# Kernel optimization log

Hardware: AMD Instinct MI355X
Metric: run time of the kernel (lower is better)

Reference implementation:

```python
import jax, jax.numpy as jnp
import numpy as np

T = 3              # num_ntype (slots)
NH = 64            # num_hidden == num_classes
HEADS = (4, 4, 1)
NUM_ETYPES = 5
EDGE_DIM = 64
N_NODES = 20000
NEG_SLOPE = 0.2
ALPHA = 0.05       # residual-attention blend
EPS = 1e-12


def _l2_by_slot(x):
    # l2_norm with l2BySlot='True': normalize each ntype slot independently
    n = x.shape[0]
    xs = x.reshape(n, T, -1)
    nrm = jnp.linalg.norm(xs, axis=2, keepdims=True)
    return (xs / jnp.maximum(nrm, EPS)).reshape(n, -1)


def _edge_softmax(logits, dst, n):
    # softmax over incoming edges of each destination node
    m = jax.lax.stop_gradient(jax.ops.segment_max(logits, dst, num_segments=n))
    e = jnp.exp(logits - m[dst])
    s = jax.ops.segment_sum(e, dst, num_segments=n)
    return e / s[dst]


def _conv(x, src, dst, etype, W, al, ar, ee_tab, We, ae, res_attn, act):
    # slotGATConv: x [N,T,C], W [T,C,H*O], al/ar [H,T*O], ee_tab [R,De], We [De,H*De], ae [H,De]
    n = x.shape[0]
    H = al.shape[0]
    proj = jnp.einsum('ntc,tcd->ntd', x, W)                     # [N,T,H*O]
    O = proj.shape[-1] // H
    feat = proj.reshape(n, T, H, O).transpose(0, 2, 1, 3).reshape(n, H, T * O)
    el = jnp.einsum('nhd,hd->nh', feat, al)
    er = jnp.einsum('nhd,hd->nh', feat, ar)
    De = ee_tab.shape[1]
    ep = (ee_tab[etype] @ We).reshape(-1, H, De)                # [E,H,De]
    ee = jnp.einsum('ehd,hd->eh', ep, ae)                       # [E,H]
    logit = jax.nn.leaky_relu(el[src] + er[dst] + ee, NEG_SLOPE)
    a = _edge_softmax(logit, dst, n)                            # [E,H]
    if res_attn is not None:
        a = a * (1.0 - ALPHA) + res_attn * ALPHA
    out = jax.ops.segment_sum(feat[src] * a[:, :, None], dst, num_segments=n)  # [N,H,T*O]
    if act:
        out = jax.nn.elu(out)
    return out, a


def _forward(feat0, feat1, feat2, w_in0, b_in0, w_in1, b_in1, w_in2, b_in2,
             l0_W, l0_al, l0_ar, l0_ee, l0_we, l0_ae,
             l1_W, l1_al, l1_ar, l1_ee, l1_we, l1_ae,
             l2_W, l2_al, l2_ar, l2_ee, l2_we, l2_ae,
             dm_W, e_feat, src, dst, left, right, mid):
    feats = [feat0, feat1, feat2]
    lins = [(w_in0, b_in0), (w_in1, b_in1), (w_in2, b_in2)]
    blocks = []
    for t, (f, (w, b)) in enumerate(zip(feats, lins)):
        ft = f @ w + b                                          # [n_t, NH]
        pad = jnp.zeros((f.shape[0], T * NH), ft.dtype)
        blocks.append(pad.at[:, t * NH:(t + 1) * NH].set(ft))   # slot zero-padding
    h = jnp.concatenate(blocks, 0)                              # [N, T*NH]
    emb = [_l2_by_slot(h)]                                      # aggregator='None' -> identity
    x = h.reshape(-1, T, NH)
    out0, a0 = _conv(x, src, dst, e_feat, l0_W, l0_al, l0_ar, l0_ee, l0_we, l0_ae, None, True)
    emb.append(_l2_by_slot(out0.mean(1)))
    x = out0.reshape(-1, HEADS[0], T, NH).transpose(0, 2, 1, 3).reshape(-1, T, HEADS[0] * NH)
    out1, a1 = _conv(x, src, dst, e_feat, l1_W, l1_al, l1_ar, l1_ee, l1_we, l1_ae, a0, True)
    emb.append(_l2_by_slot(out1.mean(1)))
    x = out1.reshape(-1, HEADS[1], T, NH).transpose(0, 2, 1, 3).reshape(-1, T, HEADS[1] * NH)
    out2, _ = _conv(x, src, dst, e_feat, l2_W, l2_al, l2_ar, l2_ee, l2_we, l2_ae, a1, False)
    emb.append(_l2_by_slot(out2.mean(1)))
    # aggregator='None' + inProcessEmb='True': concat per-slot along feature dim
    embs = [e.reshape(-1, T, NH) for e in emb]
    o = jnp.concatenate(embs, 2).reshape(-1, T * NH * len(embs))  # [N, 768]
    le, re = o[left], o[right]
    scores = jnp.zeros(left.shape[0], o.dtype)
    for r in range(NUM_ETYPES):                                 # DistMult per relation
        s = ((le @ dm_W[r]) * re).sum(1)
        scores = jnp.where(mid == r, s, scores)
    return jax.nn.sigmoid(scores)


def setup_inputs() -> dict:
    key = jax.random.key(0)
    ks = iter(jax.random.split(key, 64))
    def nrm(shape, std):
        return jax.random.normal(next(ks), shape, jnp.float32) * std
    counts = [8000, 6000, 6000]
    in_dims = [256, 128, 64]
    inp = {}
    for t in range(T):
        inp[f'feat{t}'] = jax.random.normal(next(ks), (counts[t], in_dims[t]), jnp.float32)
        inp[f'w_in{t}'] = nrm((in_dims[t], NH), 0.1)
        inp[f'b_in{t}'] = nrm((NH,), 0.1)
    Cs = [NH, HEADS[0] * NH, HEADS[1] * NH]
    for l in range(3):
        H = HEADS[l]
        inp[f'l{l}_W'] = nrm((T, Cs[l], H * NH), 0.1)
        inp[f'l{l}_al'] = nrm((H, T * NH), 0.1)
        inp[f'l{l}_ar'] = nrm((H, T * NH), 0.1)
        inp[f'l{l}_ee'] = nrm((NUM_ETYPES, EDGE_DIM), 0.1)
        inp[f'l{l}_we'] = nrm((EDGE_DIM, H * EDGE_DIM), 0.1)
        inp[f'l{l}_ae'] = nrm((H, EDGE_DIM), 0.1)
    D = T * NH * 4
    inp['dm_W'] = nrm((NUM_ETYPES, D, D), 0.05)
    E, L = 200000, 10000
    inp['e_feat'] = jax.random.randint(next(ks), (E,), 0, NUM_ETYPES)
    inp['src'] = jax.random.randint(next(ks), (E,), 0, N_NODES)
    inp['dst'] = jax.random.randint(next(ks), (E,), 0, N_NODES)
    inp['left'] = jax.random.randint(next(ks), (L,), 0, N_NODES)
    inp['right'] = jax.random.randint(next(ks), (L,), 0, N_NODES)
    inp['mid'] = jax.random.randint(next(ks), (L,), 0, NUM_ETYPES)
    return inp


def reference(feat0, feat1, feat2, w_in0, b_in0, w_in1, b_in1, w_in2, b_in2,
              l0_W, l0_al, l0_ar, l0_ee, l0_we, l0_ae,
              l1_W, l1_al, l1_ar, l1_ee, l1_we, l1_ae,
              l2_W, l2_al, l2_ar, l2_ee, l2_we, l2_ae,
              dm_W, e_feat, src, dst, left, right, mid):
    return _forward(feat0, feat1, feat2, w_in0, b_in0, w_in1, b_in1, w_in2, b_in2,
                    l0_W, l0_al, l0_ar, l0_ee, l0_we, l0_ae,
                    l1_W, l1_al, l1_ar, l1_ee, l1_we, l1_ae,
                    l2_W, l2_al, l2_ar, l2_ee, l2_we, l2_ae,
                    dm_W, e_feat, src, dst, left, right, mid)
```

## Files before the change

kernel.cpp:

```cpp
#include <hip/hip_runtime.h>
#include <math.h>

#define N_NODES 20000
#define NPAD    20096
#define N_EDGES 200000
#define N_PAIRS 10000
#define PAIR_PAD 10368
#define DM_TILES 162
#define NBLK    79

typedef __attribute__((ext_vector_type(8))) short s16x8;
typedef __attribute__((ext_vector_type(4))) float f32x4;

__device__ inline float wave_max(float v){
  for (int o = 32; o > 0; o >>= 1) v = fmaxf(v, __shfl_xor(v, o));
  return v;
}
__device__ inline float wave_sum(float v){
  for (int o = 32; o > 0; o >>= 1) v += __shfl_xor(v, o);
  return v;
}
__device__ inline short f2bf(float x){
  union { float f; unsigned u; } v; v.f = x;
  unsigned r = (v.u + 0x7FFFu + ((v.u >> 16) & 1u)) >> 16;
  return (short)r;
}
__device__ inline float bf2f(short s){
  union { unsigned u; float f; } v; v.u = ((unsigned)(unsigned short)s) << 16;
  return v.f;
}

__global__ void build_h(const float* __restrict__ f0, const float* __restrict__ w0, const float* __restrict__ b0,
                        const float* __restrict__ f1, const float* __restrict__ w1, const float* __restrict__ b1,
                        const float* __restrict__ f2, const float* __restrict__ w2, const float* __restrict__ b2,
                        short* __restrict__ Xb0, short* __restrict__ o_b,
                        int* __restrict__ csr_cnt, int* __restrict__ cnt5, int* __restrict__ pos5,
                        float* __restrict__ score, int* __restrict__ pairs,
                        float* __restrict__ eall, short* __restrict__ Xb12,
                        short* __restrict__ featb){
  const int blk = blockIdx.x, lane = threadIdx.x;
  const int gid = blk * 64 + lane;
  if (gid < N_NODES) csr_cnt[gid] = 0;
  if (gid < 5){ cnt5[gid * 16] = 0; pos5[gid * 16] = 0; }
  if (gid < 10016) score[gid] = 0.f;
  if (gid < PAIR_PAD) pairs[gid] = -1;
  for (int i = gid; i < 480000; i += 160000) eall[i] = 0.f;
  s16x8 z = {};
  if (gid < 4608){
    int t = (gid * 16) / 24576, off = (gid * 16) % 24576;
    short* p = Xb12 + ((size_t)(t * NPAD + N_NODES)) * 256 + off;
    *(s16x8*)p = z; *(s16x8*)(p + 8) = z;
  }
  if (gid < 1152){
    int t = (gid * 16) / 6144, off = (gid * 16) % 6144;
    short* p = Xb0 + ((size_t)(t * NPAD + N_NODES)) * 64 + off;
    *(s16x8*)p = z; *(s16x8*)(p + 8) = z;
  }
  int t, C, nbase; const float *f, *w, *b;
  if (blk < 1000)       { t = 0; nbase = 0;     C = 256; f = f0; w = w0; b = b0; }
  else if (blk < 1750)  { t = 1; nbase = 8000;  C = 128; f = f1; w = w1; b = b1; }
  else                  { t = 2; nbase = 14000; C = 64;  f = f2; w = w2; b = b2; }
  const int n0 = blk * 8;
  const int n0l = n0 - nbase;
  __shared__ float xs[8 * 256];
  const float* fr = f + (size_t)n0l * C;
  for (int i = lane; i < 8 * C; i += 64) xs[i] = fr[i];
  __syncthreads();
  float acc[8];
#pragma unroll
  for (int j = 0; j < 8; j++) acc[j] = b[lane];
  for (int c = 0; c < C; c++){
    float wv = w[c * 64 + lane];
#pragma unroll
    for (int j = 0; j < 8; j++) acc[j] += xs[j * C + c] * wv;
  }
  for (int j = 0; j < 8; j++){
    int n = n0 + j;
    {
      int h = lane >> 4, si = (lane >> 3) & 1, j8 = lane & 7;
      int s0 = (t == 0) ? 1 : 0;
      int s1 = (t == 2) ? 1 : 2;
      int toff = si ? s1 : s0;
      *(s16x8*)(featb + ((size_t)n * 4 + h) * 192 + toff * 64 + j8 * 8) = z;
    }
    for (int tt = 0; tt < 3; tt++)
      Xb0[((size_t)(tt * NPAD) + n) * 64 + lane] = f2bf((tt == t) ? acc[j] : 0.f);
    float ss = wave_sum(acc[j] * acc[j]);
    float sc = 1.f / fmaxf(sqrtf(ss), 1e-12f);
    for (int tt = 0; tt < 3; tt++)
      o_b[(size_t)n * 768 + tt * 256 + lane] = f2bf((tt == t) ? acc[j] * sc : 0.f);
  }
}

__global__ void count_prep_k(const int* __restrict__ dst, int* __restrict__ csr_cnt,
                             const int* __restrict__ mid, int* __restrict__ cnt5,
                             const float* __restrict__ lW0, const float* __restrict__ lW1,
                             const float* __restrict__ lW2, const float* __restrict__ dmW,
                             short* __restrict__ Wt0, short* __restrict__ Wt1,
                             short* __restrict__ Wt2, short* __restrict__ Mt,
                             const float* __restrict__ ee0, const float* __restrict__ we0, const float* __restrict__ ae0,
                             const float* __restrict__ ee1, const float* __restrict__ we1, const float* __restrict__ ae1,
                             const float* __restrict__ ee2, const float* __restrict__ we2, const float* __restrict__ ae2,
                             float* __restrict__ ee5f){
  if (blockIdx.x < 782){
    int e = blockIdx.x * 256 + threadIdx.x;
    int lane = threadIdx.x & 63;
    if (e < N_EDGES) atomicAdd(&csr_cnt[dst[e]], 1);
    int r_mine = (e < N_PAIRS) ? mid[e] : -1;
#pragma unroll
    for (int r = 0; r < 5; r++){
      unsigned long long mask = __ballot(r_mine == r);
      if (mask){
        int leader = __ffsll((long long)mask) - 1;
        if (lane == leader) atomicAdd(&cnt5[r * 16], __popcll(mask));
      }
    }
    return;
  }
  int lin = blockIdx.x - 782;
  int z = lin / 576;
  int rem = lin % 576;
  int by = rem / 24, bx = rem % 24;
  if (z == 10){
    int r = bx, L = by;
    if (r >= 5 || L >= 3) return;
    int H = (L == 2) ? 1 : 4;
    const float* eetab = (L == 0) ? ee0 : ((L == 1) ? ee1 : ee2);
    const float* We    = (L == 0) ? we0 : ((L == 1) ? we1 : we2);
    const float* ae    = (L == 0) ? ae0 : ((L == 1) ? ae1 : ae2);
    int h = threadIdx.x >> 6, lane = threadIdx.x & 63;
    if (h >= H) return;
    float v = 0.f;
    for (int k = 0; k < 64; k++) v += eetab[r * 64 + k] * We[k * H * 64 + h * 64 + lane];
    v *= ae[h * 64 + lane];
    v = wave_sum(v);
    if (lane == 0) ee5f[L * 32 + r * H + h] = v;
    return;
  }
  const float* s; short* d; int R, Cc, r0, c0;
  if (z < 5){
    s = dmW + (size_t)z * 589824; d = Mt + (size_t)z * 589824;
    R = 768; Cc = 768; r0 = bx * 32; c0 = by * 32;
  } else if (z < 8){
    if (bx >= 8 || by >= 8) return;
    int t = z - 5;
    s = lW1 + (size_t)t * 65536; d = Wt1 + (size_t)t * 65536;
    R = 256; Cc = 256; r0 = bx * 32; c0 = by * 32;
  } else if (z == 8){
    if (bx >= 6 || by >= 8) return;
    int t = bx >> 1;
    s = lW0 + (size_t)t * 16384; d = Wt0 + (size_t)t * 16384;
    R = 64; Cc = 256; r0 = (bx & 1) * 32; c0 = by * 32;
  } else {
    if (bx >= 8 || by >= 6) return;
    int t = by >> 1;
    s = lW2 + (size_t)t * 16384; d = Wt2 + (size_t)t * 16384;
    R = 256; Cc = 64; r0 = bx * 32; c0 = (by & 1) * 32;
  }
  __shared__ float tile[32][33];
  int tx = threadIdx.x & 31, ty = threadIdx.x >> 5;
  for (int i = 0; i < 32; i += 8){
    int r = r0 + ty + i;
    tile[ty + i][tx] = (r < R && c0 + tx < Cc) ? s[(size_t)r * Cc + c0 + tx] : 0.f;
  }
  __syncthreads();
  for (int i = 0; i < 32; i += 8){
    int c = c0 + ty + i;
    if (c < Cc && r0 + tx < R)
      d[(size_t)c * R + r0 + tx] = f2bf(tile[tx][ty + i]);
  }
}

__global__ void scan1_k(const int* __restrict__ cnt, int* __restrict__ loc, int* __restrict__ bsum){
  __shared__ int s[256];
  int tid = threadIdx.x;
  int idx = blockIdx.x * 256 + tid;
  int v = (idx < N_NODES) ? cnt[idx] : 0;
  s[tid] = v;
  __syncthreads();
  for (int o = 1; o < 256; o <<= 1){
    int u = (tid >= o) ? s[tid - o] : 0;
    __syncthreads();
    s[tid] += u;
    __syncthreads();
  }
  if (idx < N_NODES) loc[idx] = s[tid] - v;
  if (tid == 255) bsum[blockIdx.x] = s[255];
}

__global__ void scan2_k(const int* __restrict__ bsum, int* __restrict__ bofs,
                        const int* __restrict__ cnt5, int* __restrict__ off5){
  __shared__ int s[128];
  int tid = threadIdx.x;
  int v = (tid < NBLK) ? bsum[tid] : 0;
  s[tid] = v;
  __syncthreads();
  for (int o = 1; o < 128; o <<= 1){
    int u = (tid >= o) ? s[tid - o] : 0;
    __syncthreads();
    s[tid] += u;
    __syncthreads();
  }
  if (tid < NBLK) bofs[tid] = s[tid] - v;
  if (tid == 0){
    int r0 = 0;
    for (int r = 0; r < 5; r++){ off5[r] = r0; r0 += ((cnt5[r * 16] + 63) >> 6) << 6; }
  }
}

__global__ void scan3_k(const int* __restrict__ loc, const int* __restrict__ bofs,
                        int* __restrict__ coff, int* __restrict__ cpos){
  int idx = blockIdx.x * 256 + threadIdx.x;
  if (idx < N_NODES){
    int v = loc[idx] + bofs[blockIdx.x];
    coff[idx] = v;
    cpos[idx * 16] = v;
  }
  if (idx == 0) coff[N_NODES] = N_EDGES;
}

__global__ void scatter_k(const int* __restrict__ dst, const int* __restrict__ srcv,
                          const int* __restrict__ efeat, int* __restrict__ cpos,
                          int* __restrict__ src_sorted, int* __restrict__ et_sorted,
                          const int* __restrict__ mid, const int* __restrict__ off5,
                          int* __restrict__ pos5, int* __restrict__ pairs){
  int e = blockIdx.x * 256 + threadIdx.x;
  int lane = threadIdx.x & 63;
  if (e < N_EDGES){
    int p = atomicAdd(&cpos[dst[e] * 16], 1);
    src_sorted[p] = srcv[e];
    et_sorted[p] = efeat[e];
  }
  int r_mine = (e < N_PAIRS) ? mid[e] : -1;
#pragma unroll
  for (int r = 0; r < 5; r++){
    unsigned long long mask = __ballot(r_mine == r);
    if (mask){
      int cnt = __popcll(mask);
      int leader = __ffsll((long long)mask) - 1;
      int base = 0;
      if (lane == leader) base = atomicAdd(&pos5[r * 16], cnt);
      base = __shfl(base, leader);
      if (r_mine == r){
        int rank = __popcll(mask & ((1ull << lane) - 1ull));
        pairs[off5[r] + base + rank] = e;
      }
    }
  }
}

template<int C, int NO, int TYPED>
__global__ void mfma_proj(const short* __restrict__ Xb, const short* __restrict__ Wt,
                          short* __restrict__ featb, const float* __restrict__ al,
                          const float* __restrict__ ar, float* __restrict__ elf,
                          float* __restrict__ erf){
  constexpr int H = NO / 64;
  const int ct = blockIdx.y;
  const int t  = blockIdx.z;
  int tile = blockIdx.x;
  if (TYPED){
    const int lo[3] = {0, 62, 109};
    const int hi[3] = {63, 110, 157};
    tile += lo[t];
    if (tile >= hi[t]) return;
  }
  const int n0 = tile * 128;
  const int tid = threadIdx.x;
  const int w = tid >> 6, lane = tid & 63;
  const int quad = lane >> 4, ln = lane & 15;
  __shared__ __attribute__((aligned(16))) short A_s[128 * 32];
  __shared__ __attribute__((aligned(16))) short B_s[64 * 32];
  const short* Xt  = Xb + (size_t)t * NPAD * C;
  const short* Wtt = Wt + ((size_t)t * NO + ct * 64) * C;
  f32x4 acc[2][4] = {};
  for (int kk = 0; kk < C; kk += 32){
    {
      int row = tid >> 1, half = tid & 1;
      const s16x8* g = (const s16x8*)(Xt + (size_t)(n0 + row) * C + kk + half * 16);
      s16x8 v0 = g[0], v1 = g[1];
      *(s16x8*)(A_s + row * 32 + half * 16) = v0;
      *(s16x8*)(A_s + row * 32 + half * 16 + 8) = v1;
    }
    {
      int row = tid >> 2, chunk = tid & 3;
      s16x8 v = *(const s16x8*)(Wtt + (size_t)row * C + kk + chunk * 8);
      *(s16x8*)(B_s + row * 32 + chunk * 8) = v;
    }
    __syncthreads();
    s16x8 af0 = *(s16x8*)(A_s + (w * 32 + ln) * 32 + quad * 8);
    s16x8 af1 = *(s16x8*)(A_s + (w * 32 + 16 + ln) * 32 + quad * 8);
    s16x8 bf[4];
#pragma unroll
    for (int b = 0; b < 4; b++) bf[b] = *(s16x8*)(B_s + (b * 16 + ln) * 32 + quad * 8);
#pragma unroll
    for (int b = 0; b < 4; b++){
      acc[0][b] = __builtin_amdgcn_mfma_f32_16x16x32_bf16(af0, bf[b], acc[0][b], 0, 0, 0);
      acc[1][b] = __builtin_amdgcn_mfma_f32_16x16x32_bf16(af1, bf[b], acc[1][b], 0, 0, 0);
    }
    __syncthreads();
  }
#pragma unroll
  for (int ar_ = 0; ar_ < 2; ar_++){
#pragma unroll
    for (int i = 0; i < 4; i++){
      int n = n0 + w * 32 + ar_ * 16 + quad * 4 + i;
      if (n >= N_NODES) continue;
#pragma unroll
      for (int b = 0; b < 4; b++){
        int jj = b * 16 + ln;
        featb[((size_t)n * H + ct) * 192 + t * 64 + jj] = f2bf(acc[ar_][b][i]);
      }
    }
  }
  float alv[4], arv[4];
#pragma unroll
  for (int b = 0; b < 4; b++){
    alv[b] = al[ct * 192 + t * 64 + b * 16 + ln];
    arv[b] = ar[ct * 192 + t * 64 + b * 16 + ln];
  }
#pragma unroll
  for (int ar_ = 0; ar_ < 2; ar_++){
#pragma unroll
    for (int i = 0; i < 4; i++){
      float pe = 0.f, pr = 0.f;
#pragma unroll
      for (int b = 0; b < 4; b++){
        pe += acc[ar_][b][i] * alv[b];
        pr += acc[ar_][b][i] * arv[b];
      }
#pragma unroll
      for (int o = 1; o < 16; o <<= 1){
        pe += __shfl_xor(pe, o);
        pr += __shfl_xor(pr, o);
      }
      int n = n0 + w * 32 + ar_ * 16 + quad * 4 + i;
      if (ln == 0 && n < N_NODES){
        atomicAdd(&elf[n * H + ct], pe);
        atomicAdd(&erf[n * H + ct], pr);
      }
    }
  }
}

template<int H, int MODE, int ACT>
__global__ __launch_bounds__(256) void gat_fused(
    const int* __restrict__ csr_off, const int* __restrict__ src_sorted,
    const int* __restrict__ et_sorted,
    const float* __restrict__ el, const float* __restrict__ er, const float* __restrict__ ee5,
    const float* __restrict__ aprev, float* __restrict__ aout,
    const short* __restrict__ featb, short* __restrict__ outb,
    short* __restrict__ o_b, int kslice){
  const int wid = threadIdx.x >> 6, lane = threadIdx.x & 63;
  const int n = blockIdx.x * 4 + wid;
  if (n >= N_NODES) return;
  constexpr int NC = H * 192 / 8;
  const int c0 = lane, h0 = (c0 / 24) % H;
  const int c1 = lane + 64, h1 = (c1 / 24) % H;
  const bool act0 = (c0 < NC);
  const bool act1 = (H == 4) && (lane < 32);
  const int off = csr_off[n];
  const int cnt = csr_off[n + 1] - off;
  __shared__ float a_s[4][64][H];
  __shared__ float out_s[4][H * 192];
  float acc0[8] = {}, acc1[8] = {};
  float ern[H];
#pragma unroll
  for (int h = 0; h < H; h++) ern[h] = er[n * H + h];

  if (cnt > 0 && cnt <= 64){
    int p = off + lane;
    int sidx = 0, r = 0;
    if (lane < cnt){ sidx = src_sorted[p]; r = et_sorted[p]; }
    float lg[H];
#pragma unroll
    for (int h = 0; h < H; h++) lg[h] = -1e30f;
    if (lane < cnt){
#pragma unroll
      for (int h = 0; h < H; h++){
        float v = el[sidx * H + h] + ern[h] + ee5[r * H + h];
        lg[h] = (v >= 0.f) ? v : 0.2f * v;
      }
    }
    float ap[4] = {};
    if (MODE > 0 && lane < cnt){
#pragma unroll
      for (int q = 0; q < 4; q++) ap[q] = aprev[(size_t)p * 4 + q];
    }
    float av[H];
#pragma unroll
    for (int h = 0; h < H; h++){
      float mh = wave_max(lg[h]);
      float ex = (lane < cnt) ? __expf(lg[h] - mh) : 0.f;
      float sh = wave_sum(ex);
      float a = ex / sh;
      if (MODE == 1) a = 0.95f * a + 0.05f * ap[h];
      if (MODE == 2) a = 0.95f * a + 0.0125f * (ap[0] + ap[1] + ap[2] + ap[3]);
      av[h] = a;
      if (lane < cnt) a_s[wid][lane][h] = a;
    }
    if (MODE != 2 && lane < cnt){
      f32x4 o = {av[0], av[1], av[2], av[3]};
      *(f32x4*)(aout + (size_t)p * 4) = o;
    }
    int b = 0;
    for (; b + 4 <= cnt; b += 4){
      int p4 = off + b;
      int s0 = src_sorted[p4],     s1 = src_sorted[p4 + 1];
      int s2 = src_sorted[p4 + 2], s3 = src_sorted[p4 + 3];
      s16x8 v00, v01, v02, v03, v10, v11, v12, v13;
      if (act0){
        v00 = *(const s16x8*)(featb + (size_t)s0 * (H * 192) + c0 * 8);
        v01 = *(const s16x8*)(featb + (size_t)s1 * (H * 192) + c0 * 8);
        v02 = *(const s16x8*)(featb + (size_t)s2 * (H * 192) + c0 * 8);
        v03 = *(const s16x8*)(featb + (size_t)s3 * (H * 192) + c0 * 8);
      }
      if (act1){
        v10 = *(const s16x8*)(featb + (size_t)s0 * (H * 192) + c1 * 8);
        v11 = *(const s16x8*)(featb + (size_t)s1 * (H * 192) + c1 * 8);
        v12 = *(const s16x8*)(featb + (size_t)s2 * (H * 192) + c1 * 8);
        v13 = *(const s16x8*)(featb + (size_t)s3 * (H * 192) + c1 * 8);
      }
      if (act0){
        float a0 = a_s[wid][b][h0], a1 = a_s[wid][b + 1][h0];
        float a2 = a_s[wid][b + 2][h0], a3 = a_s[wid][b + 3][h0];
#pragma unroll
        for (int i = 0; i < 8; i++)
          acc0[i] += a0 * bf2f(v00[i]) + a1 * bf2f(v01[i]) +
                     a2 * bf2f(v02[i]) + a3 * bf2f(v03[i]);
      }
      if (act1){
        float a0 = a_s[wid][b][h1], a1 = a_s[wid][b + 1][h1];
        float a2 = a_s[wid][b + 2][h1], a3 = a_s[wid][b + 3][h1];
#pragma unroll
        for (int i = 0; i < 8; i++)
          acc1[i] += a0 * bf2f(v10[i]) + a1 * bf2f(v11[i]) +
                     a2 * bf2f(v12[i]) + a3 * bf2f(v13[i]);
      }
    }
    for (; b < cnt; b++){
      int pp = off + b;
      int s = src_sorted[pp];
      if (act0){
        float a = a_s[wid][b][h0];
        s16x8 v = *(const s16x8*)(featb + (size_t)s * (H * 192) + c0 * 8);
#pragma unroll
        for (int i = 0; i < 8; i++) acc0[i] += a * bf2f(v[i]);
      }
      if (act1){
        float a = a_s[wid][b][h1];
        s16x8 v = *(const s16x8*)(featb + (size_t)s * (H * 192) + c1 * 8);
#pragma unroll
        for (int i = 0; i < 8; i++) acc1[i] += a * bf2f(v[i]);
      }
    }
  } else if (cnt > 64){
    float mh[H], sh[H];
#pragma unroll
    for (int h = 0; h < H; h++){ mh[h] = -1e30f; sh[h] = 0.f; }
    for (int b = lane; b < cnt; b += 64){
      int p = off + b; int s = src_sorted[p]; int r = et_sorted[p];
#pragma unroll
      for (int h = 0; h < H; h++){
        float v = el[s * H + h] + ern[h] + ee5[r * H + h];
        v = (v >= 0.f) ? v : 0.2f * v;
        mh[h] = fmaxf(mh[h], v);
      }
    }
#pragma unroll
    for (int h = 0; h < H; h++) mh[h] = wave_max(mh[h]);
    for (int b = lane; b < cnt; b += 64){
      int p = off + b; int s = src_sorted[p]; int r = et_sorted[p];
#pragma unroll
      for (int h = 0; h < H; h++){
        float v = el[s * H + h] + ern[h] + ee5[r * H + h];
        v = (v >= 0.f) ? v : 0.2f * v;
        sh[h] += __expf(v - mh[h]);
      }
    }
#pragma unroll
    for (int h = 0; h < H; h++) sh[h] = wave_sum(sh[h]);
    if (MODE != 2){
      for (int b = lane; b < cnt; b += 64){
        int p = off + b; int s = src_sorted[p]; int r = et_sorted[p];
        float ap[4] = {};
        if (MODE > 0){
#pragma unroll
          for (int q = 0; q < 4; q++) ap[q] = aprev[(size_t)p * 4 + q];
        }
        float av[4] = {};
#pragma unroll
        for (int h = 0; h < H; h++){
          float v = el[s * H + h] + ern[h] + ee5[r * H + h];
          v = (v >= 0.f) ? v : 0.2f * v;
          float a = __expf(v - mh[h]) / sh[h];
          if (MODE == 1) a = 0.95f * a + 0.05f * ap[h];
          av[h] = a;
        }
        f32x4 o = {av[0], av[1], av[2], av[3]};
        *(f32x4*)(aout + (size_t)p * 4) = o;
      }
    }
    for (int b = 0; b < cnt; b++){
      int p = off + b; int s = src_sorted[p]; int r = et_sorted[p];
      const short* row = featb + (size_t)s * (H * 192);
      float apm[4] = {};
      if (MODE > 0){
#pragma unroll
        for (int q = 0; q < 4; q++) apm[q] = aprev[(size_t)p * 4 + q];
      }
      if (act0){
        float v = el[s * H + h0] + ern[h0] + ee5[r * H + h0];
        v = (v >= 0.f) ? v : 0.2f * v;
        float a = __expf(v - mh[h0]) / sh[h0];
        if (MODE == 1) a = 0.95f * a + 0.05f * apm[h0];
        if (MODE == 2) a = 0.95f * a + 0.0125f * (apm[0] + apm[1] + apm[2] + apm[3]);
        s16x8 vv = *(const s16x8*)(row + c0 * 8);
#pragma unroll
        for (int i = 0; i < 8; i++) acc0[i] += a * bf2f(vv[i]);
      }
      if (act1){
        float v = el[s * H + h1] + ern[h1] + ee5[r * H + h1];
        v = (v >= 0.f) ? v : 0.2f * v;
        float a = __expf(v - mh[h1]) / sh[h1];
        if (MODE == 1) a = 0.95f * a + 0.05f * apm[h1];
        s16x8 vv = *(const s16x8*)(row + c1 * 8);
#pragma unroll
        for (int i = 0; i < 8; i++) acc1[i] += a * bf2f(vv[i]);
      }
    }
  }
  if (act0){
    int dd = c0 * 8, h = dd / 192, rr = dd % 192, t = rr / 64, j = rr % 64;
    if (ACT){
#pragma unroll
      for (int i = 0; i < 8; i++) acc0[i] = (acc0[i] > 0.f) ? acc0[i] : expm1f(acc0[i]);
    }
#pragma unroll
    for (int i = 0; i < 8; i++) out_s[wid][dd + i] = acc0[i];
    if (outb){
      s16x8 o;
#pragma unroll
      for (int i = 0; i < 8; i++) o[i] = f2bf(acc0[i]);
      *(s16x8*)(outb + ((size_t)(t * NPAD) + n) * 256 + h * 64 + j) = o;
    }
  }
  if (act1){
    int dd = c1 * 8, h = dd / 192, rr = dd % 192, t = rr / 64, j = rr % 64;
    if (ACT){
#pragma unroll
      for (int i = 0; i < 8; i++) acc1[i] = (acc1[i] > 0.f) ? acc1[i] : expm1f(acc1[i]);
    }
#pragma unroll
    for (int i = 0; i < 8; i++) out_s[wid][dd + i] = acc1[i];
    if (outb){
      s16x8 o;
#pragma unroll
      for (int i = 0; i < 8; i++) o[i] = f2bf(acc1[i]);
      *(s16x8*)(outb + ((size_t)(t * NPAD) + n) * 256 + h * 64 + j) = o;
    }
  }
  for (int t = 0; t < 3; t++){
    float v;
    if (H == 4)
      v = 0.25f * (out_s[wid][t * 64 + lane] + out_s[wid][192 + t * 64 + lane] +
                   out_s[wid][384 + t * 64 + lane] + out_s[wid][576 + t * 64 + lane]);
    else
      v = out_s[wid][t * 64 + lane];
    float ss = wave_sum(v * v);
    float sc = 1.f / fmaxf(sqrtf(ss), 1e-12f);
    o_b[(size_t)n * 768 + t * 256 + kslice * 64 + lane] = f2bf(v * sc);
  }
}

__global__ void distmult_mfma(const short* __restrict__ o_b, const short* __restrict__ Mt,
                              const int* __restrict__ pairs, const int* __restrict__ left,
                              const int* __restrict__ right, const int* __restrict__ mid,
                              float* __restrict__ score){
  const int pt = blockIdx.x, ct = blockIdx.y;
  const int tid = threadIdx.x;
  const int w = tid >> 6, lane = tid & 63;
  const int quad = lane >> 4, ln = lane & 15;
  __shared__ __attribute__((aligned(16))) short smem[8192];
  short* A_s = smem;
  short* B_s = smem + 2048;
  __shared__ int pid_s[64];
  __shared__ int lbase[64];
  if (tid < 64){
    int p = pairs[pt * 64 + tid];
    pid_s[tid] = p;
    lbase[tid] = (p >= 0) ? left[p] * 768 : 0;
  }
  __syncthreads();
  int p0 = pid_s[0];
  if (p0 < 0) return;
  const int r = mid[p0];
  const short* Mr = Mt + (size_t)r * 768 * 768;
  f32x4 acc[8] = {};
  for (int kk = 0; kk < 768; kk += 32){
    {
      int row = tid >> 2, chunk = tid & 3;
      s16x8 v = *(const s16x8*)(o_b + (size_t)lbase[row] + kk + chunk * 8);
      *(s16x8*)(A_s + row * 32 + chunk * 8) = v;
    }
    {
      int row = tid >> 1, half = tid & 1;
      const s16x8* g = (const s16x8*)(Mr + (size_t)(ct * 128 + row) * 768 + kk + half * 16);
      s16x8 v0 = g[0], v1 = g[1];
      *(s16x8*)(B_s + row * 32 + half * 16) = v0;
      *(s16x8*)(B_s + row * 32 + half * 16 + 8) = v1;
    }
    __syncthreads();
    s16x8 af = *(s16x8*)(A_s + (w * 16 + ln) * 32 + quad * 8);
#pragma unroll
    for (int b = 0; b < 8; b++){
      s16x8 bf = *(s16x8*)(B_s + (b * 16 + ln) * 32 + quad * 8);
      acc[b] = __builtin_amdgcn_mfma_f32_16x16x32_bf16(af, bf, acc[b], 0, 0, 0);
    }
    __syncthreads();
  }
  short* RE_s = smem;
  {
    int row = tid >> 2, quarter = tid & 3;
    int p = pid_s[row];
    s16x8 v0 = {}, v1 = {}, v2 = {}, v3 = {};
    if (p >= 0){
      const s16x8* g = (const s16x8*)(o_b + (size_t)right[p] * 768 + ct * 128 + quarter * 32);
      v0 = g[0]; v1 = g[1]; v2 = g[2]; v3 = g[3];
    }
    __syncthreads();
    short* dst = RE_s + row * 128 + quarter * 32;
    *(s16x8*)(dst)      = v0;
    *(s16x8*)(dst + 8)  = v1;
    *(s16x8*)(dst + 16) = v2;
    *(s16x8*)(dst + 24) = v3;
  }
  __syncthreads();
#pragma unroll
  for (int i = 0; i < 4; i++){
    int row = w * 16 + quad * 4 + i;
    float s = 0.f;
#pragma unroll
    for (int b = 0; b < 8; b++)
      s += acc[b][i] * bf2f(RE_s[row * 128 + b * 16 + ln]);
    s += __shfl_xor(s, 1); s += __shfl_xor(s, 2);
    s += __shfl_xor(s, 4); s += __shfl_xor(s, 8);
    if (ln == 0){
      int p = pid_s[row];
      if (p >= 0) atomicAdd(&score[p], s);
    }
  }
}

__global__ void sigmoid_k(const float* __restrict__ score, float* __restrict__ out){
  int i = blockIdx.x * 256 + threadIdx.x;
  if (i < N_PAIRS) out[i] = 1.f / (1.f + __expf(-score[i]));
}

extern "C" void kernel_launch(void* const* d_in, const int* in_sizes, int n_in,
                              void* d_out, int out_size, void* d_ws, size_t ws_size,
                              hipStream_t stream){
  const float* f0 = (const float*)d_in[0];
  const float* w0 = (const float*)d_in[1];
  const float* b0 = (const float*)d_in[2];
  const float* f1 = (const float*)d_in[3];
  const float* w1 = (const float*)d_in[4];
  const float* b1 = (const float*)d_in[5];
  const float* f2 = (const float*)d_in[6];
  const float* w2_ = (const float*)d_in[7];
  const float* b2 = (const float*)d_in[8];
  const float* lW[3]  = {(const float*)d_in[9],  (const float*)d_in[15], (const float*)d_in[21]};
  const float* lal[3] = {(const float*)d_in[10], (const float*)d_in[16], (const float*)d_in[22]};
  const float* lar[3] = {(const float*)d_in[11], (const float*)d_in[17], (const float*)d_in[23]};
  const float* lee[3] = {(const float*)d_in[12], (const float*)d_in[18], (const float*)d_in[24]};
  const float* lwe[3] = {(const float*)d_in[13], (const float*)d_in[19], (const float*)d_in[25]};
  const float* lae[3] = {(const float*)d_in[14], (const float*)d_in[20], (const float*)d_in[26]};
  const float* dmW = (const float*)d_in[27];
  const int* efeat = (const int*)d_in[28];
  const int* srcv  = (const int*)d_in[29];
  const int* dstv  = (const int*)d_in[30];
  const int* left  = (const int*)d_in[31];
  const int* right = (const int*)d_in[32];
  const int* midv  = (const int*)d_in[33];
  float* out = (float*)d_out;

  short* feat_b = (short*)d_ws;
  float* aA     = (float*)(feat_b + 15360000);
  float* aB     = aA + 800000;
  float* eall   = aB + 800000;
  float* ee5f   = eall + 480000;
  float* score  = ee5f + 96;
  int* csr_cnt  = (int*)(score + 10016);
  int* csr_off  = csr_cnt + 20000;
  int* csr_pos  = csr_off + 20004;
  int* loc      = csr_pos + 320000;
  int* bsum     = loc + 20000;
  int* bofs     = bsum + 128;
  int* src_sorted = bofs + 128;
  int* et_sorted  = src_sorted + 200000;
  int* cnt5     = et_sorted + 200000;
  int* off5     = cnt5 + 80;
  int* pos5     = off5 + 8;
  int* pairs    = pos5 + 80;
  short* o_b    = (short*)(pairs + PAIR_PAD);
  short* Xb0    = o_b + 15360000;
  short* Xb12   = Xb0 + 3858432;
  short* Wt0    = Xb12 + 15433728;
  short* Wt1    = Wt0 + 49152;
  short* Wt2    = Wt1 + 196608;
  short* Mt     = Wt2 + 49152;
  float* elf0 = eall, *erf0 = eall + 80000;
  float* elf1 = eall + 160000, *erf1 = eall + 240000;
  float* elf2 = eall + 320000, *erf2 = eall + 400000;

  build_h<<<2500, 64, 0, stream>>>(f0, w0, b0, f1, w1, b1, f2, w2_, b2, Xb0, o_b,
                                   csr_cnt, cnt5, pos5, score, pairs, eall, Xb12, feat_b);
  count_prep_k<<<782 + 6336, 256, 0, stream>>>(dstv, csr_cnt, midv, cnt5,
                                               lW[0], lW[1], lW[2], dmW, Wt0, Wt1, Wt2, Mt,
                                               lee[0], lwe[0], lae[0], lee[1], lwe[1], lae[1],
                                               lee[2], lwe[2], lae[2], ee5f);
  scan1_k<<<NBLK, 256, 0, stream>>>(csr_cnt, loc, bsum);
  scan2_k<<<1, 128, 0, stream>>>(bsum, bofs, cnt5, off5);
  scan3_k<<<NBLK, 256, 0, stream>>>(loc, bofs, csr_off, csr_pos);
  scatter_k<<<782, 256, 0, stream>>>(dstv, srcv, efeat, csr_pos, src_sorted, et_sorted,
                                     midv, off5, pos5, pairs);

  { dim3 g(64, 4, 3);
    mfma_proj<64, 256, 1><<<g, 256, 0, stream>>>(Xb0, Wt0, feat_b, lal[0], lar[0], elf0, erf0); }
  gat_fused<4, 0, 1><<<5000, 256, 0, stream>>>(csr_off, src_sorted, et_sorted, elf0, erf0, ee5f,
                                               nullptr, aA, feat_b, Xb12, o_b, 1);

  { dim3 g(NPAD / 128, 4, 3);
    mfma_proj<256, 256, 0><<<g, 256, 0, stream>>>(Xb12, Wt1, feat_b, lal[1], lar[1], elf1, erf1); }
  gat_fused<4, 1, 1><<<5000, 256, 0, stream>>>(csr_off, src_sorted, et_sorted, elf1, erf1, ee5f + 32,
                                               aA, aB, feat_b, Xb12, o_b, 2);

  { dim3 g(NPAD / 128, 1, 3);
    mfma_proj<256, 64, 0><<<g, 256, 0, stream>>>(Xb12, Wt2, feat_b, lal[2], lar[2], elf2, erf2); }
  gat_fused<1, 2, 0><<<5000, 256, 0, stream>>>(csr_off, src_sorted, et_sorted, elf2, erf2, ee5f + 64,
                                               aB, nullptr, feat_b, nullptr, o_b, 3);

  { dim3 g(DM_TILES, 6); distmult_mfma<<<g, 256, 0, stream>>>(o_b, Mt, pairs, left, right, midv, score); }
  sigmoid_k<<<40, 256, 0, stream>>>(score, out);
}
```

Measured before the change: 509.3 us.

## Sort CSR edges by source node type and skip zero slots in layer-0 aggregation

Edges within each destination's CSR segment are now grouped by the source node's type, using per-(dst,type) counts and cursors. In layer 0 the projected features are nonzero only in the source's own type slot, so the typed aggregation path gathers just that 64-wide slot per head instead of all three. The other paths are also reworked: source indices are cached in shared memory, edge loops are split across half-waves and combined with cross-lane reductions, and the H=1 path is vectorised over 8 edges. Reductions and the ELU/output store are moved into a common shared-memory epilogue. The typed path depends on the node-type boundaries hardcoded at 8000 and 14000.

```diff
diff --git a/kernel.cpp b/kernel.cpp
--- a/kernel.cpp
+++ b/kernel.cpp
@@ -29,18 +29,19 @@
   union { unsigned u; float f; } v; v.u = ((unsigned)(unsigned short)s) << 16;
   return v.f;
 }
+__device__ inline int ntype(int s){ return (s < 8000) ? 0 : ((s < 14000) ? 1 : 2); }
 
 __global__ void build_h(const float* __restrict__ f0, const float* __restrict__ w0, const float* __restrict__ b0,
                         const float* __restrict__ f1, const float* __restrict__ w1, const float* __restrict__ b1,
                         const float* __restrict__ f2, const float* __restrict__ w2, const float* __restrict__ b2,
                         short* __restrict__ Xb0, short* __restrict__ o_b,
-                        int* __restrict__ csr_cnt, int* __restrict__ cnt5, int* __restrict__ pos5,
+                        int* __restrict__ cnt3, int* __restrict__ cnt5, int* __restrict__ pos5,
                         float* __restrict__ score, int* __restrict__ pairs,
                         float* __restrict__ eall, short* __restrict__ Xb12,
                         short* __restrict__ featb){
   const int blk = blockIdx.x, lane = threadIdx.x;
   const int gid = blk * 64 + lane;
-  if (gid < N_NODES) csr_cnt[gid] = 0;
+  if (gid < 80000) cnt3[gid] = 0;
   if (gid < 5){ cnt5[gid * 16] = 0; pos5[gid * 16] = 0; }
   if (gid < 10016) score[gid] = 0.f;
   if (gid < PAIR_PAD) pairs[gid] = -1;
@@ -92,7 +93,8 @@
   }
 }
 
-__global__ void count_prep_k(const int* __restrict__ dst, int* __restrict__ csr_cnt,
+__global__ void count_prep_k(const int* __restrict__ dst, const int* __restrict__ srcv,
+                             int* __restrict__ cnt3,
                              const int* __restrict__ mid, int* __restrict__ cnt5,
                              const float* __restrict__ lW0, const float* __restrict__ lW1,
                              const float* __restrict__ lW2, const float* __restrict__ dmW,
@@ -105,7 +107,10 @@
   if (blockIdx.x < 782){
     int e = blockIdx.x * 256 + threadIdx.x;
     int lane = threadIdx.x & 63;
-    if (e < N_EDGES) atomicAdd(&csr_cnt[dst[e]], 1);
+    if (e < N_EDGES){
+      int tt = ntype(srcv[e]);
+      atomicAdd(&cnt3[dst[e] * 4 + tt], 1);
+    }
     int r_mine = (e < N_PAIRS) ? mid[e] : -1;
 #pragma unroll
     for (int r = 0; r < 5; r++){
@@ -171,11 +176,11 @@
   }
 }
 
-__global__ void scan1_k(const int* __restrict__ cnt, int* __restrict__ loc, int* __restrict__ bsum){
+__global__ void scan1_k(const int* __restrict__ cnt3, int* __restrict__ loc, int* __restrict__ bsum){
   __shared__ int s[256];
   int tid = threadIdx.x;
   int idx = blockIdx.x * 256 + tid;
-  int v = (idx < N_NODES) ? cnt[idx] : 0;
+  int v = (idx < N_NODES) ? (cnt3[idx * 4] + cnt3[idx * 4 + 1] + cnt3[idx * 4 + 2]) : 0;
   s[tid] = v;
   __syncthreads();
   for (int o = 1; o < 256; o <<= 1){
@@ -209,12 +214,16 @@
 }
 
 __global__ void scan3_k(const int* __restrict__ loc, const int* __restrict__ bofs,
-                        int* __restrict__ coff, int* __restrict__ cpos){
+                        int* __restrict__ coff, int* __restrict__ cpos,
+                        const int* __restrict__ cnt3){
   int idx = blockIdx.x * 256 + threadIdx.x;
   if (idx < N_NODES){
     int v = loc[idx] + bofs[blockIdx.x];
     coff[idx] = v;
-    cpos[idx * 16] = v;
+    int c0 = cnt3[idx * 4], c1 = cnt3[idx * 4 + 1];
+    cpos[idx * 4]     = v;
+    cpos[idx * 4 + 1] = v + c0;
+    cpos[idx * 4 + 2] = v + c0 + c1;
   }
   if (idx == 0) coff[N_NODES] = N_EDGES;
 }
@@ -227,8 +236,10 @@
   int e = blockIdx.x * 256 + threadIdx.x;
   int lane = threadIdx.x & 63;
   if (e < N_EDGES){
-    int p = atomicAdd(&cpos[dst[e] * 16], 1);
-    src_sorted[p] = srcv[e];
+    int s = srcv[e];
+    int tt = ntype(s);
+    int p = atomicAdd(&cpos[dst[e] * 4 + tt], 1);
+    src_sorted[p] = s;
     et_sorted[p] = efeat[e];
   }
   int r_mine = (e < N_PAIRS) ? mid[e] : -1;
@@ -342,35 +353,32 @@
   }
 }
 
-template<int H, int MODE, int ACT>
+template<int H, int MODE, int ACT, int TYPED>
 __global__ __launch_bounds__(256) void gat_fused(
     const int* __restrict__ csr_off, const int* __restrict__ src_sorted,
     const int* __restrict__ et_sorted,
     const float* __restrict__ el, const float* __restrict__ er, const float* __restrict__ ee5,
     const float* __restrict__ aprev, float* __restrict__ aout,
     const short* __restrict__ featb, short* __restrict__ outb,
-    short* __restrict__ o_b, int kslice){
+    short* __restrict__ o_b, const int* __restrict__ cnt3, int kslice){
   const int wid = threadIdx.x >> 6, lane = threadIdx.x & 63;
   const int n = blockIdx.x * 4 + wid;
   if (n >= N_NODES) return;
-  constexpr int NC = H * 192 / 8;
-  const int c0 = lane, h0 = (c0 / 24) % H;
-  const int c1 = lane + 64, h1 = (c1 / 24) % H;
-  const bool act0 = (c0 < NC);
-  const bool act1 = (H == 4) && (lane < 32);
   const int off = csr_off[n];
   const int cnt = csr_off[n + 1] - off;
   __shared__ float a_s[4][64][H];
+  __shared__ int   src_s[4][64];
   __shared__ float out_s[4][H * 192];
-  float acc0[8] = {}, acc1[8] = {};
   float ern[H];
 #pragma unroll
   for (int h = 0; h < H; h++) ern[h] = er[n * H + h];
 
-  if (cnt > 0 && cnt <= 64){
+  if (cnt <= 64){
     int p = off + lane;
     int sidx = 0, r = 0;
     if (lane < cnt){ sidx = src_sorted[p]; r = et_sorted[p]; }
+    int src0 = (cnt > 0) ? src_sorted[off] : 0;
+    src_s[wid][lane] = (lane < cnt) ? sidx : src0;
     float lg[H];
 #pragma unroll
     for (int h = 0; h < H; h++) lg[h] = -1e30f;
@@ -396,64 +404,104 @@
       if (MODE == 1) a = 0.95f * a + 0.05f * ap[h];
       if (MODE == 2) a = 0.95f * a + 0.0125f * (ap[0] + ap[1] + ap[2] + ap[3]);
       av[h] = a;
-      if (lane < cnt) a_s[wid][lane][h] = a;
-    }
-    if (MODE != 2 && lane < cnt){
-      f32x4 o = {av[0], av[1], av[2], av[3]};
-      *(f32x4*)(aout + (size_t)p * 4) = o;
-    }
-    int b = 0;
-    for (; b + 4 <= cnt; b += 4){
-      int p4 = off + b;
-      int s0 = src_sorted[p4],     s1 = src_sorted[p4 + 1];
-      int s2 = src_sorted[p4 + 2], s3 = src_sorted[p4 + 3];
-      s16x8 v00, v01, v02, v03, v10, v11, v12, v13;
-      if (act0){
-        v00 = *(const s16x8*)(featb + (size_t)s0 * (H * 192) + c0 * 8);
-        v01 = *(const s16x8*)(featb + (size_t)s1 * (H * 192) + c0 * 8);
-        v02 = *(const s16x8*)(featb + (size_t)s2 * (H * 192) + c0 * 8);
-        v03 = *(const s16x8*)(featb + (size_t)s3 * (H * 192) + c0 * 8);
-      }
-      if (act1){
-        v10 = *(const s16x8*)(featb + (size_t)s0 * (H * 192) + c1 * 8);
-        v11 = *(const s16x8*)(featb + (size_t)s1 * (H * 192) + c1 * 8);
-        v12 = *(const s16x8*)(featb + (size_t)s2 * (H * 192) + c1 * 8);
-        v13 = *(const s16x8*)(featb + (size_t)s3 * (H * 192) + c1 * 8);
-      }
-      if (act0){
-        float a0 = a_s[wid][b][h0], a1 = a_s[wid][b + 1][h0];
-        float a2 = a_s[wid][b + 2][h0], a3 = a_s[wid][b + 3][h0];
-#pragma unroll
-        for (int i = 0; i < 8; i++)
-          acc0[i] += a0 * bf2f(v00[i]) + a1 * bf2f(v01[i]) +
-                     a2 * bf2f(v02[i]) + a3 * bf2f(v03[i]);
-      }
-      if (act1){
-        float a0 = a_s[wid][b][h1], a1 = a_s[wid][b + 1][h1];
-        float a2 = a_s[wid][b + 2][h1], a3 = a_s[wid][b + 3][h1];
-#pragma unroll
-        for (int i = 0; i < 8; i++)
-          acc1[i] += a0 * bf2f(v10[i]) + a1 * bf2f(v11[i]) +
-                     a2 * bf2f(v12[i]) + a3 * bf2f(v13[i]);
-      }
-    }
-    for (; b < cnt; b++){
-      int pp = off + b;
-      int s = src_sorted[pp];
-      if (act0){
-        float a = a_s[wid][b][h0];
-        s16x8 v = *(const s16x8*)(featb + (size_t)s * (H * 192) + c0 * 8);
-#pragma unroll
-        for (int i = 0; i < 8; i++) acc0[i] += a * bf2f(v[i]);
-      }
-      if (act1){
-        float a = a_s[wid][b][h1];
-        s16x8 v = *(const s16x8*)(featb + (size_t)s * (H * 192) + c1 * 8);
-#pragma unroll
-        for (int i = 0; i < 8; i++) acc1[i] += a * bf2f(v[i]);
-      }
-    }
-  } else if (cnt > 64){
+      a_s[wid][lane][h] = (lane < cnt) ? a : 0.f;
+    }
+    if constexpr (MODE != 2){
+      if (lane < cnt){
+        f32x4 o = {av[0], av[1], av[2], av[3]};
+        *(f32x4*)(aout + (size_t)p * 4) = o;
+      }
+    }
+
+    if constexpr (TYPED && H == 4){
+      const int q = lane & 31, eo = lane >> 5;
+      const int hh = q >> 3, j8 = q & 7;
+      float acc[3][8] = {};
+      const int b1 = cnt3[n * 4], b2 = b1 + cnt3[n * 4 + 1];
+      const int rb[4] = {0, b1, b2, cnt};
+#pragma unroll
+      for (int t = 0; t < 3; t++){
+        for (int b = rb[t]; b < rb[t + 1]; b += 2){
+          int e = b + eo;
+          bool vld = e < rb[t + 1];
+          int ei = vld ? e : rb[t + 1] - 1;
+          int s = src_s[wid][ei];
+          float a = vld ? a_s[wid][ei][hh] : 0.f;
+          s16x8 fv = *(const s16x8*)(featb + ((size_t)s * 4 + hh) * 192 + t * 64 + j8 * 8);
+#pragma unroll
+          for (int i = 0; i < 8; i++) acc[t][i] += a * bf2f(fv[i]);
+        }
+      }
+#pragma unroll
+      for (int t = 0; t < 3; t++){
+#pragma unroll
+        for (int i = 0; i < 8; i++){
+          float tot = acc[t][i] + __shfl_xor(acc[t][i], 32);
+          if (lane < 32) out_s[wid][(hh * 24 + t * 8 + j8) * 8 + i] = tot;
+        }
+      }
+    } else if constexpr (H == 4){
+      const int p0 = lane;
+      const int p1 = (lane < 32) ? lane + 64 : lane - 32;
+      const int p2 = lane + 32;
+      const int hA = p0 / 24, hB = p1 / 24, hC = p2 / 24;
+      float acc0[8] = {}, acc1[8] = {}, acc2[8] = {};
+      const int cnt2 = (cnt + 1) & ~1;
+      for (int b = 0; b < cnt2; b += 2){
+        int eB = b + (lane >> 5), eC = b + 1;
+        int sA = src_s[wid][b], sB = src_s[wid][eB], sC = src_s[wid][eC];
+        float aA = a_s[wid][b][hA];
+        float aB = a_s[wid][eB][hB];
+        float aC = a_s[wid][eC][hC];
+        s16x8 fA = *(const s16x8*)(featb + (size_t)sA * 768 + p0 * 8);
+        s16x8 fB = *(const s16x8*)(featb + (size_t)sB * 768 + p1 * 8);
+        s16x8 fC = *(const s16x8*)(featb + (size_t)sC * 768 + p2 * 8);
+#pragma unroll
+        for (int i = 0; i < 8; i++){
+          acc0[i] += aA * bf2f(fA[i]);
+          acc1[i] += aB * bf2f(fB[i]);
+          acc2[i] += aC * bf2f(fC[i]);
+        }
+      }
+#pragma unroll
+      for (int i = 0; i < 8; i++){
+        float v1 = (lane < 32) ? acc2[i] : acc1[i];
+        float r1 = __shfl_xor(v1, 32);
+        out_s[wid][p0 * 8 + i] = acc0[i] + r1;
+        float r2 = __shfl_xor(acc2[i], 32);
+        if (lane < 32) out_s[wid][p1 * 8 + i] = acc1[i] + r2;
+      }
+    } else {
+      const int eo = lane & 7, cb = lane >> 3;
+      float acc[3][8] = {};
+      for (int b = 0; b < cnt; b += 8){
+        int e = b + eo;
+        float a = a_s[wid][e][0];
+        int s = src_s[wid][e];
+#pragma unroll
+        for (int c = 0; c < 3; c++){
+          s16x8 fv = *(const s16x8*)(featb + (size_t)s * 192 + (cb * 3 + c) * 8);
+#pragma unroll
+          for (int i = 0; i < 8; i++) acc[c][i] += a * bf2f(fv[i]);
+        }
+      }
+#pragma unroll
+      for (int c = 0; c < 3; c++){
+#pragma unroll
+        for (int i = 0; i < 8; i++){
+          float v = acc[c][i];
+          v += __shfl_xor(v, 1); v += __shfl_xor(v, 2); v += __shfl_xor(v, 4);
+          if (eo == 0) out_s[wid][(cb * 3 + c) * 8 + i] = v;
+        }
+      }
+    }
+  } else {
+    constexpr int NC = H * 192 / 8;
+    const int c0 = lane, h0 = (c0 / 24) % H;
+    const int c1 = lane + 64, h1 = (c1 / 24) % H;
+    const bool act0 = (c0 < NC);
+    const bool act1 = (H == 4) && (lane < 32);
+    float acc0[8] = {}, acc1[8] = {};
     float mh[H], sh[H];
 #pragma unroll
     for (int h = 0; h < H; h++){ mh[h] = -1e30f; sh[h] = 0.f; }
@@ -528,35 +576,61 @@
         for (int i = 0; i < 8; i++) acc1[i] += a * bf2f(vv[i]);
       }
     }
-  }
-  if (act0){
-    int dd = c0 * 8, h = dd / 192, rr = dd % 192, t = rr / 64, j = rr % 64;
-    if (ACT){
-#pragma unroll
-      for (int i = 0; i < 8; i++) acc0[i] = (acc0[i] > 0.f) ? acc0[i] : expm1f(acc0[i]);
-    }
-#pragma unroll
-    for (int i = 0; i < 8; i++) out_s[wid][dd + i] = acc0[i];
-    if (outb){
-      s16x8 o;
-#pragma unroll
-      for (int i = 0; i < 8; i++) o[i] = f2bf(acc0[i]);
-      *(s16x8*)(outb + ((size_t)(t * NPAD) + n) * 256 + h * 64 + j) = o;
-    }
-  }
-  if (act1){
-    int dd = c1 * 8, h = dd / 192, rr = dd % 192, t = rr / 64, j = rr % 64;
-    if (ACT){
-#pragma unroll
-      for (int i = 0; i < 8; i++) acc1[i] = (acc1[i] > 0.f) ? acc1[i] : expm1f(acc1[i]);
-    }
-#pragma unroll
-    for (int i = 0; i < 8; i++) out_s[wid][dd + i] = acc1[i];
-    if (outb){
-      s16x8 o;
-#pragma unroll
-      for (int i = 0; i < 8; i++) o[i] = f2bf(acc1[i]);
-      *(s16x8*)(outb + ((size_t)(t * NPAD) + n) * 256 + h * 64 + j) = o;
+    if (act0){
+#pragma unroll
+      for (int i = 0; i < 8; i++) out_s[wid][c0 * 8 + i] = acc0[i];
+    }
+    if (act1){
+#pragma unroll
+      for (int i = 0; i < 8; i++) out_s[wid][c1 * 8 + i] = acc1[i];
+    }
+  }
+
+  constexpr int NC = H * 192 / 8;
+  {
+    const int c0 = lane;
+    if (c0 < NC){
+      float v[8];
+#pragma unroll
+      for (int i = 0; i < 8; i++) v[i] = out_s[wid][c0 * 8 + i];
+      if (ACT){
+#pragma unroll
+        for (int i = 0; i < 8; i++) v[i] = (v[i] > 0.f) ? v[i] : expm1f(v[i]);
+      }
+      if (outb){
+        int dd = c0 * 8, h = dd / 192, rr = dd % 192, t = rr / 64, j = rr % 64;
+        s16x8 o;
+#pragma unroll
+        for (int i = 0; i < 8; i++) o[i] = f2bf(v[i]);
+        *(s16x8*)(outb + ((size_t)(t * NPAD) + n) * 256 + h * 64 + j) = o;
+      }
+      if (ACT){
+#pragma unroll
+        for (int i = 0; i < 8; i++) out_s[wid][c0 * 8 + i] = v[i];
+      }
+    }
+    if constexpr (H == 4){
+      if (lane < 32){
+        const int c1 = lane + 64;
+        float v[8];
+#pragma unroll
+        for (int i = 0; i < 8; i++) v[i] = out_s[wid][c1 * 8 + i];
+        if (ACT){
+#pragma unroll
+          for (int i = 0; i < 8; i++) v[i] = (v[i] > 0.f) ? v[i] : expm1f(v[i]);
+        }
+        if (outb){
+          int dd = c1 * 8, h = dd / 192, rr = dd % 192, t = rr / 64, j = rr % 64;
+          s16x8 o;
+#pragma unroll
+          for (int i = 0; i < 8; i++) o[i] = f2bf(v[i]);
+          *(s16x8*)(outb + ((size_t)(t * NPAD) + n) * 256 + h * 64 + j) = o;
+        }
+        if (ACT){
+#pragma unroll
+          for (int i = 0; i < 8; i++) out_s[wid][c1 * 8 + i] = v[i];
+        }
+      }
     }
   }
   for (int t = 0; t < 3; t++){
@@ -689,10 +763,10 @@
   float* eall   = aB + 800000;
   float* ee5f   = eall + 480000;
   float* score  = ee5f + 96;
-  int* csr_cnt  = (int*)(score + 10016);
-  int* csr_off  = csr_cnt + 20000;
+  int* cnt3     = (int*)(score + 10016);
+  int* csr_off  = cnt3 + 80000;
   int* csr_pos  = csr_off + 20004;
-  int* loc      = csr_pos + 320000;
+  int* loc      = csr_pos + 80000;
   int* bsum     = loc + 20000;
   int* bofs     = bsum + 128;
   int* src_sorted = bofs + 128;
@@ -713,31 +787,31 @@
   float* elf2 = eall + 320000, *erf2 = eall + 400000;
 
   build_h<<<2500, 64, 0, stream>>>(f0, w0, b0, f1, w1, b1, f2, w2_, b2, Xb0, o_b,
-                                   csr_cnt, cnt5, pos5, score, pairs, eall, Xb12, feat_b);
-  count_prep_k<<<782 + 6336, 256, 0, stream>>>(dstv, csr_cnt, midv, cnt5,
+                                   cnt3, cnt5, pos5, score, pairs, eall, Xb12, feat_b);
+  count_prep_k<<<782 + 6336, 256, 0, stream>>>(dstv, srcv, cnt3, midv, cnt5,
                                                lW[0], lW[1], lW[2], dmW, Wt0, Wt1, Wt2, Mt,
                                                lee[0], lwe[0], lae[0], lee[1], lwe[1], lae[1],
                                                lee[2], lwe[2], lae[2], ee5f);
-  scan1_k<<<NBLK, 256, 0, stream>>>(csr_cnt, loc, bsum);
+  scan1_k<<<NBLK, 256, 0, stream>>>(cnt3, loc, bsum);
   scan2_k<<<1, 128, 0, stream>>>(bsum, bofs, cnt5, off5);
-  scan3_k<<<NBLK, 256, 0, stream>>>(loc, bofs, csr_off, csr_pos);
+  scan3_k<<<NBLK, 256, 0, stream>>>(loc, bofs, csr_off, csr_pos, cnt3);
   scatter_k<<<782, 256, 0, stream>>>(dstv, srcv, efeat, csr_pos, src_sorted, et_sorted,
                                      midv, off5, pos5, pairs);
 
   { dim3 g(64, 4, 3);
     mfma_proj<64, 256, 1><<<g, 256, 0, stream>>>(Xb0, Wt0, feat_b, lal[0], lar[0], elf0, erf0); }
-  gat_fused<4, 0, 1><<<5000, 256, 0, stream>>>(csr_off, src_sorted, et_sorted, elf0, erf0, ee5f,
-                                               nullptr, aA, feat_b, Xb12, o_b, 1);
+  gat_fused<4, 0, 1, 1><<<5000, 256, 0, stream>>>(csr_off, src_sorted, et_sorted, elf0, erf0, ee5f,
+                                                  nullptr, aA, feat_b, Xb12, o_b, cnt3, 1);
 
   { dim3 g(NPAD / 128, 4, 3);
     mfma_proj<256, 256, 0><<<g, 256, 0, stream>>>(Xb12, Wt1, feat_b, lal[1], lar[1], elf1, erf1); }
-  gat_fused<4, 1, 1><<<5000, 256, 0, stream>>>(csr_off, src_sorted, et_sorted, elf1, erf1, ee5f + 32,
-                                               aA, aB, feat_b, Xb12, o_b, 2);
+  gat_fused<4, 1, 1, 0><<<5000, 256, 0, stream>>>(csr_off, src_sorted, et_sorted, elf1, erf1, ee5f + 32,
+                                                  aA, aB, feat_b, Xb12, o_b, cnt3, 2);
 
   { dim3 g(NPAD / 128, 1, 3);
     mfma_proj<256, 64, 0><<<g, 256, 0, stream>>>(Xb12, Wt2, feat_b, lal[2], lar[2], elf2, erf2); }
-  gat_fused<1, 2, 0><<<5000, 256, 0, stream>>>(csr_off, src_sorted, et_sorted, elf2, erf2, ee5f + 64,
-                                               aB, nullptr, feat_b, nullptr, o_b, 3);
+  gat_fused<1, 2, 0, 0><<<5000, 256, 0, stream>>>(csr_off, src_sorted, et_sorted, elf2, erf2, ee5f + 64,
+                                                  aB, nullptr, feat_b, nullptr, o_b, cnt3, 3);
 
   { dim3 g(DM_TILES, 6); distmult_mfma<<<g, 256, 0, stream>>>(o_b, Mt, pairs, left, right, midv, score); }
   sigmoid_k<<<40, 256, 0, stream>>>(score, out);
```

New measurement: 469.9 us. -7.7%, faster.
